# Kernel tuning notes

Hardware: AMD Instinct MI355X
Metric: run time of the kernel (lower is better)

## Reference

```python
import jax, jax.numpy as jnp
import numpy as np

D_MODEL = 1024
NUM_HEADS = 16
D_KEY = D_MODEL // NUM_HEADS


def setup_inputs() -> dict:
    key = jax.random.key(0)
    ks = jax.random.split(key, 9)
    B, S = 2, 2048
    s = 1.0 / np.sqrt(D_MODEL)
    return {
        "x": jax.random.normal(ks[0], (B, S, D_MODEL), dtype=jnp.float32),
        "W_q": jax.random.normal(ks[1], (D_MODEL, D_MODEL), dtype=jnp.float32) * s,
        "b_q": jnp.zeros((D_MODEL,), dtype=jnp.float32),
        "W_k": jax.random.normal(ks[2], (D_MODEL, D_MODEL), dtype=jnp.float32) * s,
        "b_k": jnp.zeros((D_MODEL,), dtype=jnp.float32),
        "W_v": jax.random.normal(ks[3], (D_MODEL, D_MODEL), dtype=jnp.float32) * s,
        "b_v": jnp.zeros((D_MODEL,), dtype=jnp.float32),
        "W_o": jax.random.normal(ks[4], (D_MODEL, D_MODEL), dtype=jnp.float32) * s,
        "b_o": jnp.zeros((D_MODEL,), dtype=jnp.float32),
    }


def reference(x, W_q, b_q, W_k, b_k, W_v, b_v, W_o, b_o):
    B, S, _ = x.shape
    # Linear projections (torch nn.Linear: x @ W.T + b; here W stored as [in, out])
    Q = x @ W_q + b_q
    K = x @ W_k + b_k
    V = x @ W_v + b_v
    # [B, S, H, dk] -> [B, H, S, dk]
    def split_heads(t):
        return t.reshape(B, S, NUM_HEADS, D_KEY).transpose(0, 2, 1, 3)
    Q, K, V = split_heads(Q), split_heads(K), split_heads(V)
    scale = 1.0 / np.sqrt(D_KEY).astype(np.float32)
    logits = jnp.einsum("bhqd,bhkd->bhqk", Q, K) * scale  # [B,H,S,S]
    weights = jax.nn.softmax(logits, axis=-1)
    ctx = jnp.einsum("bhqk,bhkd->bhqd", weights, V)       # [B,H,S,dk]
    concat = ctx.transpose(0, 2, 1, 3).reshape(B, S, D_MODEL)
    return concat @ W_o + b_o
```

## Files before the change

### kernel.cpp

```cpp
#include <hip/hip_runtime.h>
#include <cstdint>
#include <cstddef>

#define SEQ   2048
#define NH    16
#define DK    64
#define DM    1024
#define MTOT  4096
#define QSCALE (0.125f * 1.44269504088896f)

typedef __attribute__((ext_vector_type(8))) short           short8;
typedef __attribute__((ext_vector_type(8))) unsigned short  ushort8;
typedef __attribute__((ext_vector_type(4))) unsigned short  ushort4v;
typedef __attribute__((ext_vector_type(2))) unsigned int    uint2v;
typedef __attribute__((ext_vector_type(4))) unsigned int    uint4v;
typedef __attribute__((ext_vector_type(4))) float           float4v;
typedef unsigned short u16;
typedef unsigned int   u32;

__device__ inline float4v mfma16(short8 a, short8 b, float4v c) {
    return __builtin_amdgcn_mfma_f32_16x16x32_bf16(a, b, c, 0, 0, 0);
}
__device__ inline u16 f2bf(float f) {
    u32 u = __float_as_uint(f);
    u += 0x7fffu + ((u >> 16) & 1u);
    return (u16)(u >> 16);
}
__device__ inline u32 pkbf(float a, float b) {
    u32 r;
    asm("v_cvt_pk_bf16_f32 %0, %1, %2" : "=v"(r) : "v"(a), "v"(b));
    return r;
}
__device__ inline float ex2(float x) {
    float r;
    asm("v_exp_f32 %0, %1" : "=v"(r) : "v"(x));
    return r;
}
__device__ inline void pl32swap(u32& a, u32& b) {
    asm("v_permlane32_swap_b32 %0, %1" : "+v"(a), "+v"(b));
}
__device__ inline void pl16swap(u32& a, u32& b) {
    asm("v_permlane16_swap_b32 %0, %1" : "+v"(a), "+v"(b));
}
__device__ inline void gld16(const void* g, void* lds) {
    __builtin_amdgcn_global_load_lds(
        (const __attribute__((address_space(1))) u32*)g,
        (__attribute__((address_space(3))) u32*)lds, 16, 0, 0);
}

__global__ __launch_bounds__(256)
void convert_x(const float* __restrict__ x, u16* __restrict__ xb)
{
    const int i = blockIdx.x * 256 + threadIdx.x;
    const float4v a = ((const float4v*)x)[2 * i];
    const float4v b = ((const float4v*)x)[2 * i + 1];
    ushort8 o;
    #pragma unroll
    for (int j = 0; j < 4; j++) { o[j] = f2bf(a[j]); o[4 + j] = f2bf(b[j]); }
    ((ushort8*)xb)[i] = o;
}

__global__ __launch_bounds__(256)
void transpose_w(const float* __restrict__ W0, const float* __restrict__ W1,
                 const float* __restrict__ W2, const float* __restrict__ W3,
                 u16* __restrict__ T0, u16* __restrict__ T1,
                 u16* __restrict__ T2, u16* __restrict__ T3)
{
    __shared__ u16 t[64][68];
    const float* W; u16* T;
    switch (blockIdx.z) {
        case 0: W = W0; T = T0; break;
        case 1: W = W1; T = T1; break;
        case 2: W = W2; T = T2; break;
        default: W = W3; T = T3; break;
    }
    const int n0 = blockIdx.x * 64, k0 = blockIdx.y * 64;
    const int r  = threadIdx.x >> 4;
    const int c4 = (threadIdx.x & 15) * 4;
    #pragma unroll
    for (int i = 0; i < 4; i++) {
        float4v v = *(const float4v*)&W[(size_t)(k0 + r + i * 16) * DM + n0 + c4];
        #pragma unroll
        for (int j = 0; j < 4; j++) t[r + i * 16][c4 + j] = f2bf(v[j]);
    }
    __syncthreads();
    #pragma unroll
    for (int i = 0; i < 4; i++) {
        const int rr = r + i * 16;
        ushort4v o;
        #pragma unroll
        for (int j = 0; j < 4; j++) o[j] = t[c4 + j][rr];
        *(ushort4v*)&T[(size_t)(n0 + rr) * DM + k0 + c4] = o;
    }
}

template<int TM, int MODE>
__global__ __launch_bounds__(512)
void gemm_bt(const u16* __restrict__ A, const u16* __restrict__ WT,
             const float* __restrict__ bq, const float* __restrict__ bk,
             const float* __restrict__ bv,
             void* __restrict__ out0, u16* __restrict__ outK, u16* __restrict__ outV)
{
    constexpr int NT = 512;
    constexpr int MF = TM / 32;
    __shared__ u16 Al[TM][64];
    __shared__ u16 Bl[128][64];
    const int tid  = threadIdx.x;
    const int lane = tid & 63, w = tid >> 6;
    const int quad = lane >> 4, l16 = lane & 15;

    const int nxb  = gridDim.x;
    const int wgid = blockIdx.y * nxb + blockIdx.x;
    const int per  = (nxb * gridDim.y) >> 3;
    const int nl   = (wgid & 7) * per + (wgid >> 3);
    const int n0 = (nl % nxb) * 128, m0 = (nl / nxb) * TM;

    const int wm = (w >> 2) * (TM / 2);
    const int wn = (w & 3) * 32;

    float4v acc[MF][2] = {};

    for (int k0 = 0; k0 < DM; k0 += 64) {
        __syncthreads();
        #pragma unroll
        for (int j = 0; j < TM * 8 / NT; j++) {
            const int c = j * NT + tid;
            const int row = c >> 3, kc = c & 7;
            gld16(A + (size_t)(m0 + row) * DM + k0 + ((kc ^ (row & 7)) * 8),
                  &Al[0][0] + (size_t)(j * NT + w * 64) * 8);
        }
        #pragma unroll
        for (int j = 0; j < 1024 / NT; j++) {
            const int c = j * NT + tid;
            const int row = c >> 3, kc = c & 7;
            gld16(WT + (size_t)(n0 + row) * DM + k0 + ((kc ^ (row & 7)) * 8),
                  &Bl[0][0] + (size_t)(j * NT + w * 64) * 8);
        }
        __syncthreads();
        #pragma unroll
        for (int u = 0; u < 2; u++) {
            short8 af[MF], bf[2];
            #pragma unroll
            for (int mi = 0; mi < MF; mi++) {
                const int row = wm + mi * 16 + l16;
                af[mi] = *(const short8*)&Al[row][((4 * u + quad) ^ (row & 7)) * 8];
            }
            #pragma unroll
            for (int ni = 0; ni < 2; ni++) {
                const int row = wn + ni * 16 + l16;
                bf[ni] = *(const short8*)&Bl[row][((4 * u + quad) ^ (row & 7)) * 8];
            }
            #pragma unroll
            for (int mi = 0; mi < MF; mi++)
                #pragma unroll
                for (int ni = 0; ni < 2; ni++)
                    acc[mi][ni] = mfma16(af[mi], bf[ni], acc[mi][ni]);
        }
    }

    if constexpr (MODE == 0) {
        float* out = (float*)out0;
        #pragma unroll
        for (int ni = 0; ni < 2; ni++) {
            const int col = n0 + wn + ni * 16 + l16;
            const float bb = bq[col];
            #pragma unroll
            for (int mi = 0; mi < MF; mi++)
                #pragma unroll
                for (int r = 0; r < 4; r++) {
                    const int row = m0 + wm + mi * 16 + quad * 4 + r;
                    out[(size_t)row * DM + col] = acc[mi][ni][r] + bb;
                }
        }
    } else {
        const int seg = n0 >> 10;
        u16* outp = (seg == 0) ? (u16*)out0 : (seg == 1 ? outK : outV);
        const float* bias = (seg == 0) ? bq : (seg == 1 ? bk : bv);
        const float scl = (seg == 0) ? QSCALE : 1.0f;
        if (seg < 2) {
            #pragma unroll
            for (int ni = 0; ni < 2; ni++) {
                const int col = (n0 & 1023) + wn + ni * 16 + l16;
                const float bb = bias[col];
                const int h = col >> 6, d = col & 63;
                #pragma unroll
                for (int mi = 0; mi < MF; mi++)
                    #pragma unroll
                    for (int r = 0; r < 4; r++) {
                        const int row = m0 + wm + mi * 16 + quad * 4 + r;
                        const int b = row >> 11, s = row & (SEQ - 1);
                        outp[(((size_t)(b * NH + h) * SEQ + s) << 6) + d] =
                            f2bf((acc[mi][ni][r] + bb) * scl);
                    }
            }
        } else {
            #pragma unroll
            for (int ni = 0; ni < 2; ni++) {
                const int col = (n0 & 1023) + wn + ni * 16 + l16;
                const float bb = bias[col];
                const int h = col >> 6, d = col & 63;
                #pragma unroll
                for (int mi = 0; mi < MF; mi++) {
                    const int row0 = m0 + wm + mi * 16 + quad * 4;
                    const int b = row0 >> 11, s = row0 & (SEQ - 1);
                    uint2v pv;
                    pv[0] = pkbf(acc[mi][ni][0] + bb, acc[mi][ni][1] + bb);
                    pv[1] = pkbf(acc[mi][ni][2] + bb, acc[mi][ni][3] + bb);
                    *(uint2v*)&outp[(((size_t)((b * NH + h) * DK + d)) << 11) + s] = pv;
                }
            }
        }
    }
}

__global__ __launch_bounds__(512, 4)
void attn_kernel(const u16* __restrict__ Q, const u16* __restrict__ K,
                 const u16* __restrict__ VT, u16* __restrict__ Ctx)
{
    __shared__ __align__(16) u16 pool[32768];

    const int tid  = threadIdx.x;
    const int lane = tid & 63, w = tid >> 6;
    const int wq = w & 3, wgrp = w >> 2;
    const int quad = lane >> 4, l16 = lane & 15;

    const int wgid = blockIdx.y * 16 + blockIdx.x;
    const int nlin = (wgid & 7) * 64 + (wgid >> 3);
    const int qt = nlin & 15;
    const int bh = nlin >> 4;
    const size_t head = (size_t)bh * SEQ * DK;

    short8 qf[2][2];
    #pragma unroll
    for (int g = 0; g < 2; g++) {
        const size_t qrow = head + (size_t)(qt * 128 + wq * 32 + g * 16 + l16) * DK;
        qf[g][0] = *(const short8*)(Q + qrow + quad * 8);
        qf[g][1] = *(const short8*)(Q + qrow + 32 + quad * 8);
    }

    float4v acc[2][4] = {};
    float l_part[2] = {0.f, 0.f};

    const int sh = tid >> 8;
    const int rK = (tid >> 3) & 31, cK = tid & 7;
    const int dV = (tid >> 2) & 63, cV = tid & 3;
    const int sVk = (dV & 3) ^ ((dV >> 2) & 3);
    const u16* const Kg = K  + head + (size_t)(sh * 1024 + rK) * DK + (cK ^ (rK & 7)) * 8;
    const u16* const Vg = VT + head + (size_t)dV * SEQ + sh * 1024 + (cV ^ sVk) * 8;
    u16* const Kdst = pool + tid * 8;
    u16* const Vdst = pool + 16384 + tid * 8;

    auto QKSTEP = [&](int cur, float4v znew[2][2]) {
        short8 kf[2][2];
        #pragma unroll
        for (int t = 0; t < 2; t++) {
            const int row = t * 16 + l16;
            const u16* kb = pool + cur * 4096 + wgrp * 2048 + row * 64;
            kf[t][0] = *(const short8*)(kb + (quad ^ (row & 7)) * 8);
            kf[t][1] = *(const short8*)(kb + ((4 + quad) ^ (row & 7)) * 8);
        }
        __builtin_amdgcn_s_setprio(1);
        #pragma unroll
        for (int t = 0; t < 2; t++)
            #pragma unroll
            for (int g = 0; g < 2; g++) {
                float4v zz = {};
                zz = mfma16(kf[t][0], qf[g][0], zz);
                zz = mfma16(kf[t][1], qf[g][1], zz);
                znew[t][g] = zz;
            }
        __builtin_amdgcn_s_setprio(0);
    };

    auto SMPACK = [&](float4v zp[2][2], short8 pf[2]) {
        #pragma unroll
        for (int g = 0; g < 2; g++) {
            float p[2][4];
            #pragma unroll
            for (int t = 0; t < 2; t++) {
                p[t][0] = ex2(zp[t][g][0]); p[t][1] = ex2(zp[t][g][1]);
                p[t][2] = ex2(zp[t][g][2]); p[t][3] = ex2(zp[t][g][3]);
                l_part[g] += (p[t][0] + p[t][1]) + (p[t][2] + p[t][3]);
            }
            u32 A = pkbf(p[0][0], p[0][1]);
            u32 B = pkbf(p[0][2], p[0][3]);
            u32 C = pkbf(p[1][0], p[1][1]);
            u32 D = pkbf(p[1][2], p[1][3]);
            pl32swap(A, C); pl16swap(A, C);
            pl32swap(B, D); pl16swap(B, D);
            uint4v pw; pw[0] = A; pw[1] = B; pw[2] = C; pw[3] = D;
            pf[g] = __builtin_bit_cast(short8, pw);
        }
    };

    auto PVSTEP = [&](int pv, short8 pf[2]) {
        __builtin_amdgcn_s_setprio(1);
        #pragma unroll
        for (int t = 0; t < 4; t++) {
            const int d = t * 16 + l16;
            const u16* vb = pool + 16384 + pv * 4096 + wgrp * 2048 + d * 32;
            const short8 vf =
                *(const short8*)(vb + (quad ^ ((d & 3) ^ ((d >> 2) & 3))) * 8);
            acc[0][t] = mfma16(vf, pf[0], acc[0][t]);
            acc[1][t] = mfma16(vf, pf[1], acc[1][t]);
        }
        __builtin_amdgcn_s_setprio(0);
    };

    gld16(Kg,                 Kdst);
    gld16(Vg,                 Vdst);
    gld16(Kg + 32 * DK,       Kdst + 4096);
    gld16(Vg + 32,            Vdst + 4096);

    float4v zp[2][2];

    __syncthreads();
    gld16(Kg + (size_t)2 * 32 * DK, Kdst + 2 * 4096);
    gld16(Vg + (size_t)2 * 32,      Vdst + 2 * 4096);
    QKSTEP(0, zp);

    for (int it = 1; it < 32; ++it) {
        const int cur = it & 3, pv = (it - 1) & 3;
        __syncthreads();
        if (it + 2 < 32) {
            gld16(Kg + (size_t)(it + 2) * 32 * DK, Kdst + ((it + 2) & 3) * 4096);
            gld16(Vg + (size_t)(it + 2) * 32,      Vdst + ((it + 2) & 3) * 4096);
        }
        float4v zn[2][2];
        QKSTEP(cur, zn);
        short8 pf[2];
        SMPACK(zp, pf);
        PVSTEP(pv, pf);
        #pragma unroll
        for (int t = 0; t < 2; t++)
            #pragma unroll
            for (int g = 0; g < 2; g++) zp[t][g] = zn[t][g];
    }
    {
        short8 pf[2];
        SMPACK(zp, pf);
        PVSTEP(3, pf);
    }

    #pragma unroll
    for (int g = 0; g < 2; g++) {
        l_part[g] += __shfl_xor(l_part[g], 16);
        l_part[g] += __shfl_xor(l_part[g], 32);
    }

    float* const Xlp = (float*)pool;
    #define XL(a, b, c) Xlp[(((a) * 64 + (b)) * 17) + (c)]
    float ltot[2];
    #pragma unroll
    for (int p = 0; p < 2; p++) {
        __syncthreads();
        if (wgrp == 1) {
            #pragma unroll
            for (int g = 0; g < 2; g++)
                #pragma unroll
                for (int tt = 0; tt < 2; tt++)
                    #pragma unroll
                    for (int r = 0; r < 4; r++)
                        XL(wq, lane, g * 8 + tt * 4 + r) = acc[g][2 * p + tt][r];
            XL(wq, lane, 16) = l_part[p];
        }
        __syncthreads();
        if (wgrp == 0) {
            #pragma unroll
            for (int g = 0; g < 2; g++)
                #pragma unroll
                for (int tt = 0; tt < 2; tt++)
                    #pragma unroll
                    for (int r = 0; r < 4; r++)
                        acc[g][2 * p + tt][r] += XL(wq, lane, g * 8 + tt * 4 + r);
            ltot[p] = l_part[p] + XL(wq, lane, 16);
        }
    }
    #undef XL

    if (wgrp == 0) {
        const int b = bh >> 4, h = bh & 15;
        #pragma unroll
        for (int g = 0; g < 2; g++) {
            const float rl = 1.0f / ltot[g];
            const int s = qt * 128 + wq * 32 + g * 16 + l16;
            u16* dst = Ctx + (size_t)(b * SEQ + s) * DM + h * 64 + quad * 4;
            #pragma unroll
            for (int t = 0; t < 4; t++) {
                uint2v ov;
                ov[0] = pkbf(acc[g][t][0] * rl, acc[g][t][1] * rl);
                ov[1] = pkbf(acc[g][t][2] * rl, acc[g][t][3] * rl);
                *(uint2v*)&dst[t * 16] = ov;
            }
        }
    }
}

extern "C" void kernel_launch(void* const* d_in, const int* in_sizes, int n_in,
                              void* d_out, int out_size, void* d_ws, size_t ws_size,
                              hipStream_t stream)
{
    const float* x   = (const float*)d_in[0];
    const float* W_q = (const float*)d_in[1];
    const float* b_q = (const float*)d_in[2];
    const float* W_k = (const float*)d_in[3];
    const float* b_k = (const float*)d_in[4];
    const float* W_v = (const float*)d_in[5];
    const float* b_v = (const float*)d_in[6];
    const float* W_o = (const float*)d_in[7];
    const float* b_o = (const float*)d_in[8];

    u16* xb  = (u16*)d_ws;
    u16* WT  = xb + (size_t)MTOT * DM;
    u16* WTo = WT + (size_t)3 * DM * DM;
    u16* VTb = WTo + (size_t)DM * DM;
    u16* Cb  = xb;
    u16* Qb  = (u16*)d_out;
    u16* Kb  = Qb + (size_t)MTOT * DM;

    convert_x<<<2048, 256, 0, stream>>>(x, xb);
    transpose_w<<<dim3(16, 16, 4), 256, 0, stream>>>(
        W_q, W_k, W_v, W_o, WT, WT + (size_t)DM * DM, WT + (size_t)2 * DM * DM, WTo);
    gemm_bt<128, 1><<<dim3(24, 32), 512, 0, stream>>>(xb, WT, b_q, b_k, b_v, Qb, Kb, VTb);
    attn_kernel<<<dim3(SEQ / 128, 2 * NH), 512, 0, stream>>>(Qb, Kb, VTb, Cb);
    gemm_bt<64, 0><<<dim3(8, 64), 512, 0, stream>>>(Cb, WTo, b_o, nullptr, nullptr,
                                                    (float*)d_out, nullptr, nullptr);
}
```

Before: 185.1 us.

## Drop split-K wave groups in attention; use 64-query tiles with 256 threads

The attention kernel no longer splits the key sequence across two wave groups that are then reduced through shared memory. Each workgroup now handles 64 queries with 4 waves, each wave covering 16 query rows across all 2048 keys, and the grid doubles to 1024 blocks. This removes the final LDS reduction and its barriers and halves LDS per block, which should allow more resident blocks. In exchange each K/V tile loaded into LDS is reused by fewer queries, so global and LDS traffic per query doubles, and the serial loop is twice as long.

```diff
diff --git a/kernel.cpp b/kernel.cpp
--- a/kernel.cpp
+++ b/kernel.cpp
@@ -213,185 +213,137 @@
     }
 }
 
-__global__ __launch_bounds__(512, 4)
+__global__ __launch_bounds__(256, 4)
 void attn_kernel(const u16* __restrict__ Q, const u16* __restrict__ K,
                  const u16* __restrict__ VT, u16* __restrict__ Ctx)
 {
-    __shared__ __align__(16) u16 pool[32768];
+    __shared__ __align__(16) u16 pool[16384];
 
     const int tid  = threadIdx.x;
     const int lane = tid & 63, w = tid >> 6;
-    const int wq = w & 3, wgrp = w >> 2;
     const int quad = lane >> 4, l16 = lane & 15;
 
-    const int wgid = blockIdx.y * 16 + blockIdx.x;
-    const int nlin = (wgid & 7) * 64 + (wgid >> 3);
-    const int qt = nlin & 15;
-    const int bh = nlin >> 4;
+    const int wgid = blockIdx.y * 32 + blockIdx.x;
+    const int nlin = (wgid & 7) * 128 + (wgid >> 3);
+    const int qt = nlin & 31;
+    const int bh = nlin >> 5;
     const size_t head = (size_t)bh * SEQ * DK;
 
-    short8 qf[2][2];
-    #pragma unroll
-    for (int g = 0; g < 2; g++) {
-        const size_t qrow = head + (size_t)(qt * 128 + wq * 32 + g * 16 + l16) * DK;
-        qf[g][0] = *(const short8*)(Q + qrow + quad * 8);
-        qf[g][1] = *(const short8*)(Q + qrow + 32 + quad * 8);
-    }
-
-    float4v acc[2][4] = {};
-    float l_part[2] = {0.f, 0.f};
-
-    const int sh = tid >> 8;
-    const int rK = (tid >> 3) & 31, cK = tid & 7;
-    const int dV = (tid >> 2) & 63, cV = tid & 3;
+    short8 qf[2];
+    {
+        const size_t qrow = head + (size_t)(qt * 64 + w * 16 + l16) * DK;
+        qf[0] = *(const short8*)(Q + qrow + quad * 8);
+        qf[1] = *(const short8*)(Q + qrow + 32 + quad * 8);
+    }
+
+    float4v acc[4] = {};
+    float l_part = 0.f;
+
+    const int rK = tid >> 3, cK = tid & 7;
+    const int dV = tid >> 2, cV = tid & 3;
     const int sVk = (dV & 3) ^ ((dV >> 2) & 3);
-    const u16* const Kg = K  + head + (size_t)(sh * 1024 + rK) * DK + (cK ^ (rK & 7)) * 8;
-    const u16* const Vg = VT + head + (size_t)dV * SEQ + sh * 1024 + (cV ^ sVk) * 8;
+    const u16* const Kg = K  + head + (size_t)rK * DK + (cK ^ (rK & 7)) * 8;
+    const u16* const Vg = VT + head + (size_t)dV * SEQ + (cV ^ sVk) * 8;
     u16* const Kdst = pool + tid * 8;
-    u16* const Vdst = pool + 16384 + tid * 8;
-
-    auto QKSTEP = [&](int cur, float4v znew[2][2]) {
+    u16* const Vdst = pool + 8192 + tid * 8;
+
+    auto QKSTEP = [&](int cur, float4v znew[2]) {
         short8 kf[2][2];
         #pragma unroll
         for (int t = 0; t < 2; t++) {
             const int row = t * 16 + l16;
-            const u16* kb = pool + cur * 4096 + wgrp * 2048 + row * 64;
+            const u16* kb = pool + cur * 2048 + row * 64;
             kf[t][0] = *(const short8*)(kb + (quad ^ (row & 7)) * 8);
             kf[t][1] = *(const short8*)(kb + ((4 + quad) ^ (row & 7)) * 8);
         }
         __builtin_amdgcn_s_setprio(1);
         #pragma unroll
-        for (int t = 0; t < 2; t++)
-            #pragma unroll
-            for (int g = 0; g < 2; g++) {
-                float4v zz = {};
-                zz = mfma16(kf[t][0], qf[g][0], zz);
-                zz = mfma16(kf[t][1], qf[g][1], zz);
-                znew[t][g] = zz;
-            }
+        for (int t = 0; t < 2; t++) {
+            float4v zz = {};
+            zz = mfma16(kf[t][0], qf[0], zz);
+            zz = mfma16(kf[t][1], qf[1], zz);
+            znew[t] = zz;
+        }
         __builtin_amdgcn_s_setprio(0);
     };
 
-    auto SMPACK = [&](float4v zp[2][2], short8 pf[2]) {
-        #pragma unroll
-        for (int g = 0; g < 2; g++) {
-            float p[2][4];
-            #pragma unroll
-            for (int t = 0; t < 2; t++) {
-                p[t][0] = ex2(zp[t][g][0]); p[t][1] = ex2(zp[t][g][1]);
-                p[t][2] = ex2(zp[t][g][2]); p[t][3] = ex2(zp[t][g][3]);
-                l_part[g] += (p[t][0] + p[t][1]) + (p[t][2] + p[t][3]);
-            }
-            u32 A = pkbf(p[0][0], p[0][1]);
-            u32 B = pkbf(p[0][2], p[0][3]);
-            u32 C = pkbf(p[1][0], p[1][1]);
-            u32 D = pkbf(p[1][2], p[1][3]);
-            pl32swap(A, C); pl16swap(A, C);
-            pl32swap(B, D); pl16swap(B, D);
-            uint4v pw; pw[0] = A; pw[1] = B; pw[2] = C; pw[3] = D;
-            pf[g] = __builtin_bit_cast(short8, pw);
-        }
+    auto SMPACK = [&](float4v zp[2], short8& pf) {
+        float p[2][4];
+        #pragma unroll
+        for (int t = 0; t < 2; t++) {
+            p[t][0] = ex2(zp[t][0]); p[t][1] = ex2(zp[t][1]);
+            p[t][2] = ex2(zp[t][2]); p[t][3] = ex2(zp[t][3]);
+            l_part += (p[t][0] + p[t][1]) + (p[t][2] + p[t][3]);
+        }
+        u32 A = pkbf(p[0][0], p[0][1]);
+        u32 B = pkbf(p[0][2], p[0][3]);
+        u32 C = pkbf(p[1][0], p[1][1]);
+        u32 D = pkbf(p[1][2], p[1][3]);
+        pl32swap(A, C); pl16swap(A, C);
+        pl32swap(B, D); pl16swap(B, D);
+        uint4v pw; pw[0] = A; pw[1] = B; pw[2] = C; pw[3] = D;
+        pf = __builtin_bit_cast(short8, pw);
     };
 
-    auto PVSTEP = [&](int pv, short8 pf[2]) {
+    auto PVSTEP = [&](int pv, short8 pf) {
         __builtin_amdgcn_s_setprio(1);
         #pragma unroll
         for (int t = 0; t < 4; t++) {
             const int d = t * 16 + l16;
-            const u16* vb = pool + 16384 + pv * 4096 + wgrp * 2048 + d * 32;
+            const u16* vb = pool + 8192 + pv * 2048 + d * 32;
             const short8 vf =
                 *(const short8*)(vb + (quad ^ ((d & 3) ^ ((d >> 2) & 3))) * 8);
-            acc[0][t] = mfma16(vf, pf[0], acc[0][t]);
-            acc[1][t] = mfma16(vf, pf[1], acc[1][t]);
+            acc[t] = mfma16(vf, pf, acc[t]);
         }
         __builtin_amdgcn_s_setprio(0);
     };
 
     gld16(Kg,                 Kdst);
     gld16(Vg,                 Vdst);
-    gld16(Kg + 32 * DK,       Kdst + 4096);
-    gld16(Vg + 32,            Vdst + 4096);
-
-    float4v zp[2][2];
+    gld16(Kg + 32 * DK,       Kdst + 2048);
+    gld16(Vg + 32,            Vdst + 2048);
+
+    float4v zp[2];
 
     __syncthreads();
-    gld16(Kg + (size_t)2 * 32 * DK, Kdst + 2 * 4096);
-    gld16(Vg + (size_t)2 * 32,      Vdst + 2 * 4096);
+    gld16(Kg + (size_t)2 * 32 * DK, Kdst + 2 * 2048);
+    gld16(Vg + (size_t)2 * 32,      Vdst + 2 * 2048);
     QKSTEP(0, zp);
 
-    for (int it = 1; it < 32; ++it) {
+    for (int it = 1; it < 64; ++it) {
         const int cur = it & 3, pv = (it - 1) & 3;
         __syncthreads();
-        if (it + 2 < 32) {
-            gld16(Kg + (size_t)(it + 2) * 32 * DK, Kdst + ((it + 2) & 3) * 4096);
-            gld16(Vg + (size_t)(it + 2) * 32,      Vdst + ((it + 2) & 3) * 4096);
-        }
-        float4v zn[2][2];
+        if (it + 2 < 64) {
+            gld16(Kg + (size_t)(it + 2) * 32 * DK, Kdst + ((it + 2) & 3) * 2048);
+            gld16(Vg + (size_t)(it + 2) * 32,      Vdst + ((it + 2) & 3) * 2048);
+        }
+        float4v zn[2];
         QKSTEP(cur, zn);
-        short8 pf[2];
+        short8 pf;
         SMPACK(zp, pf);
         PVSTEP(pv, pf);
-        #pragma unroll
-        for (int t = 0; t < 2; t++)
-            #pragma unroll
-            for (int g = 0; g < 2; g++) zp[t][g] = zn[t][g];
+        zp[0] = zn[0]; zp[1] = zn[1];
     }
     {
-        short8 pf[2];
+        short8 pf;
         SMPACK(zp, pf);
         PVSTEP(3, pf);
     }
 
-    #pragma unroll
-    for (int g = 0; g < 2; g++) {
-        l_part[g] += __shfl_xor(l_part[g], 16);
-        l_part[g] += __shfl_xor(l_part[g], 32);
-    }
-
-    float* const Xlp = (float*)pool;
-    #define XL(a, b, c) Xlp[(((a) * 64 + (b)) * 17) + (c)]
-    float ltot[2];
-    #pragma unroll
-    for (int p = 0; p < 2; p++) {
-        __syncthreads();
-        if (wgrp == 1) {
-            #pragma unroll
-            for (int g = 0; g < 2; g++)
-                #pragma unroll
-                for (int tt = 0; tt < 2; tt++)
-                    #pragma unroll
-                    for (int r = 0; r < 4; r++)
-                        XL(wq, lane, g * 8 + tt * 4 + r) = acc[g][2 * p + tt][r];
-            XL(wq, lane, 16) = l_part[p];
-        }
-        __syncthreads();
-        if (wgrp == 0) {
-            #pragma unroll
-            for (int g = 0; g < 2; g++)
-                #pragma unroll
-                for (int tt = 0; tt < 2; tt++)
-                    #pragma unroll
-                    for (int r = 0; r < 4; r++)
-                        acc[g][2 * p + tt][r] += XL(wq, lane, g * 8 + tt * 4 + r);
-            ltot[p] = l_part[p] + XL(wq, lane, 16);
-        }
-    }
-    #undef XL
-
-    if (wgrp == 0) {
+    l_part += __shfl_xor(l_part, 16);
+    l_part += __shfl_xor(l_part, 32);
+
+    {
         const int b = bh >> 4, h = bh & 15;
-        #pragma unroll
-        for (int g = 0; g < 2; g++) {
-            const float rl = 1.0f / ltot[g];
-            const int s = qt * 128 + wq * 32 + g * 16 + l16;
-            u16* dst = Ctx + (size_t)(b * SEQ + s) * DM + h * 64 + quad * 4;
-            #pragma unroll
-            for (int t = 0; t < 4; t++) {
-                uint2v ov;
-                ov[0] = pkbf(acc[g][t][0] * rl, acc[g][t][1] * rl);
-                ov[1] = pkbf(acc[g][t][2] * rl, acc[g][t][3] * rl);
-                *(uint2v*)&dst[t * 16] = ov;
-            }
+        const float rl = 1.0f / l_part;
+        const int s = qt * 64 + w * 16 + l16;
+        u16* dst = Ctx + (size_t)(b * SEQ + s) * DM + h * 64 + quad * 4;
+        #pragma unroll
+        for (int t = 0; t < 4; t++) {
+            uint2v ov;
+            ov[0] = pkbf(acc[t][0] * rl, acc[t][1] * rl);
+            ov[1] = pkbf(acc[t][2] * rl, acc[t][3] * rl);
+            *(uint2v*)&dst[t * 16] = ov;
         }
     }
 }
@@ -422,7 +374,7 @@
     transpose_w<<<dim3(16, 16, 4), 256, 0, stream>>>(
         W_q, W_k, W_v, W_o, WT, WT + (size_t)DM * DM, WT + (size_t)2 * DM * DM, WTo);
     gemm_bt<128, 1><<<dim3(24, 32), 512, 0, stream>>>(xb, WT, b_q, b_k, b_v, Qb, Kb, VTb);
-    attn_kernel<<<dim3(SEQ / 128, 2 * NH), 512, 0, stream>>>(Qb, Kb, VTb, Cb);
+    attn_kernel<<<dim3(32, 32), 256, 0, stream>>>(Qb, Kb, VTb, Cb);
     gemm_bt<64, 0><<<dim3(8, 64), 512, 0, stream>>>(Cb, WTo, b_o, nullptr, nullptr,
                                                     (float*)d_out, nullptr, nullptr);
 }
```

Result: no change. 188.4 us (+1.8%).
